# Kernel optimization log

Measured on AMD Instinct MI355X. Metric: run time of the kernel, lower is better.

## Reference

```python
import jax, jax.numpy as jnp
import numpy as np

N_SENTS, N_ENTS, BATCH, DIM, HEADS = 64, 16, 64, 512, 8


def setup_inputs() -> dict:
    key = jax.random.key(0)
    ks = jax.random.split(key, 10)
    se = N_SENTS * N_ENTS
    s = 0.02  # init scale for projection weights
    entities = jax.random.normal(ks[0], (se, BATCH, DIM), dtype=jnp.float32)
    query_param = jax.random.uniform(ks[1], (1, 1, DIM), jnp.float32, -1.0, 1.0)
    wq = jax.random.normal(ks[2], (DIM, DIM), jnp.float32) * s
    wk = jax.random.normal(ks[3], (DIM, DIM), jnp.float32) * s
    wv = jax.random.normal(ks[4], (DIM, DIM), jnp.float32) * s
    wo = jax.random.normal(ks[5], (DIM, DIM), jnp.float32) * s
    bq = jax.random.normal(ks[6], (DIM,), jnp.float32) * s
    bk = jax.random.normal(ks[7], (DIM,), jnp.float32) * s
    bv = jax.random.normal(ks[8], (DIM,), jnp.float32) * s
    bo = jax.random.normal(ks[9], (DIM,), jnp.float32) * s
    return {"entities": entities, "query_param": query_param,
            "wq": wq, "wk": wk, "wv": wv, "wo": wo,
            "bq": bq, "bk": bk, "bv": bv, "bo": bo,
            "n_sents": N_SENTS}


def reference(entities, query_param, wq, wk, wv, wo, bq, bk, bv, bo, n_sents):
    # entities: [n_sents*n_ents, batch, dim]
    se, b, d = entities.shape
    n_ents = se // n_sents
    h = HEADS
    hd = d // h

    # Learned single query broadcast to every (sentence, batch) slot.
    q_in = jnp.broadcast_to(query_param, (n_sents, b, d))
    q = q_in @ wq.T + bq            # [n_sents, b, d]
    k = entities @ wk.T + bk        # [se, b, d]
    v = entities @ wv.T + bv        # [se, b, d]

    # Split heads -> [b, h, len, hd]
    qh = q.reshape(n_sents, b, h, hd).transpose(1, 2, 0, 3)
    kh = k.reshape(se, b, h, hd).transpose(1, 2, 0, 3)
    vh = v.reshape(se, b, h, hd).transpose(1, 2, 0, 3)

    scale = jnp.asarray(1.0 / np.sqrt(hd), dtype=qh.dtype)
    scores = jnp.einsum('bhqd,bhkd->bhqk', qh, kh) * scale  # [b,h,n_sents,se]

    # Block-diagonal mask: query i attends only to keys [i*n_ents, (i+1)*n_ents)
    valid = (jnp.arange(se) // n_ents)[None, :] == jnp.arange(n_sents)[:, None]
    scores = jnp.where(valid[None, None], scores, jnp.finfo(scores.dtype).min)

    attn = jax.nn.softmax(scores, axis=-1)
    ctx = jnp.einsum('bhqk,bhkd->bhqd', attn, vh)            # [b,h,n_sents,hd]
    out = ctx.transpose(2, 0, 1, 3).reshape(n_sents, b, d)   # merge heads
    return out @ wo.T + bo                                   # [n_sents, b, d]
```

## Files before the change

kernel.cpp:

```cpp
#include <hip/hip_runtime.h>
#include <stdint.h>

#define HEADS 8
#define DIM   512
#define HD    64
#define NE    16
#define NS    64
#define NB    64

typedef short bf16x8 __attribute__((ext_vector_type(8)));
typedef float f32x4  __attribute__((ext_vector_type(4)));

__device__ __forceinline__ unsigned short f2bf(float f) {
    union { float f; uint32_t u; } v; v.f = f;
    uint32_t u = v.u;
    u += 0x7fffu + ((u >> 16) & 1u);
    return (unsigned short)(u >> 16);
}
__device__ __forceinline__ float bf_lo(uint32_t u) {
    union { uint32_t u; float f; } v; v.u = u << 16; return v.f;
}
__device__ __forceinline__ float bf_hi(uint32_t u) {
    union { uint32_t u; float f; } v; v.u = u & 0xffff0000u; return v.f;
}

__device__ __forceinline__ uint32_t cvt2(float a, float b) {
    uint32_t r;
    asm("v_cvt_pk_bf16_f32 %0, %1, %2" : "=v"(r) : "v"(a), "v"(b));
    return r;
}
__device__ __forceinline__ uint2 cvt4(float4 v) {
    return (uint2){cvt2(v.x, v.y), cvt2(v.z, v.w)};
}

__global__ __launch_bounds__(256) void k_prep(
    const float* __restrict__ qp, const float* __restrict__ wq,
    const float* __restrict__ bq, const float* __restrict__ wk,
    const float* __restrict__ wv, const float* __restrict__ wo,
    unsigned short* __restrict__ u_bf,
    unsigned short* __restrict__ wv_bf, unsigned short* __restrict__ wo_bf)
{
    const int bid = blockIdx.x;
    const int t = threadIdx.x;
    if (bid < 16) {
        const int h = bid >> 1, ch = bid & 1;
        __shared__ float qs[HD];
        {
            const int j = t >> 2, q = t & 3;
            const float* w = wq + (size_t)(h * HD + j) * DIM + q * 128;
            const float* qq = qp + q * 128;
            float a = 0.f;
            #pragma unroll 8
            for (int i = 0; i < 128; i++) a += w[i] * qq[i];
            a += __shfl_xor(a, 1);
            a += __shfl_xor(a, 2);
            if (q == 0) qs[j] = a + bq[h * HD + j];
        }
        __syncthreads();
        const int c = ch * 256 + t;
        const float* w = wk + (size_t)(h * HD) * DIM + c;
        float acc = 0.f;
        #pragma unroll 8
        for (int j = 0; j < HD; j++) acc += qs[j] * w[(size_t)j * DIM];
        u_bf[h * DIM + c] = f2bf(acc);
        u_bf[(h + 8) * DIM + c] = 0;
        return;
    }
    const bool is_v = bid < 272;
    const float* src = is_v ? wv : wo;
    unsigned short* dst = is_v ? wv_bf : wo_bf;
    const int li = ((is_v ? bid - 16 : bid - 272) * 1024 + t * 4);
    const float4 v = *(const float4*)(src + li);
    ushort4 hv;
    hv.x = f2bf(v.x); hv.y = f2bf(v.y); hv.z = f2bf(v.z); hv.w = f2bf(v.w);
    *(ushort4*)(dst + li) = hv;
}

__global__ __launch_bounds__(256, 6) void k_attn(
    const float* __restrict__ ents, const unsigned short* __restrict__ u_bf,
    unsigned short* __restrict__ weighted)
{
    __shared__ unsigned short ent[NE * DIM];
    __shared__ float attn_s[NE][8];
    const int t = threadIdx.x;
    const int bid = blockIdx.x;
    const int s = bid >> 6, b = bid & 63;

    {
        const float* base = ents + ((size_t)(s * NE) * NB + b) * DIM;
        float4 v[8];
        #pragma unroll
        for (int i = 0; i < 8; i++) {
            const int c = t + 256 * i;
            const int e = c >> 7, d4 = c & 127;
            v[i] = *(const float4*)(base + (size_t)e * (NB * DIM) + (d4 << 2));
        }
        #pragma unroll
        for (int i = 0; i < 8; i++) {
            const int c = t + 256 * i;
            const int e = c >> 7, d4 = c & 127;
            const uint2 hv = cvt4(v[i]);
            const uint32_t off = (uint32_t)((e << 10) | (d4 << 3)) ^ (uint32_t)((e & 7) << 4);
            *(uint2*)((char*)ent + off) = hv;
        }
    }
    __syncthreads();

    if (t < 64) {
        const int m = t & 15, g = t >> 4;
        const uint32_t swz = (uint32_t)((m & 7) << 4);
        const uint32_t rowb = (uint32_t)(m << 10);
        const unsigned short* urow = u_bf + m * DIM + g * 8;
        f32x4 acc = {0.f, 0.f, 0.f, 0.f};
        #pragma unroll
        for (int ks = 0; ks < 16; ks++) {
            const int kp = g * 8 + ks * 32;
            const bf16x8 af = *(const bf16x8*)((const char*)ent + ((rowb + (uint32_t)(kp << 1)) ^ swz));
            const bf16x8 bf = *(const bf16x8*)(urow + ks * 32);
            acc = __builtin_amdgcn_mfma_f32_16x16x32_bf16(af, bf, acc, 0, 0, 0);
        }
        const float scale = 0.125f;
        float s0 = acc[0]*scale, s1 = acc[1]*scale, s2 = acc[2]*scale, s3 = acc[3]*scale;
        float mx = fmaxf(fmaxf(s0, s1), fmaxf(s2, s3));
        mx = fmaxf(mx, __shfl_xor(mx, 16));
        mx = fmaxf(mx, __shfl_xor(mx, 32));
        const float p0 = __expf(s0 - mx), p1 = __expf(s1 - mx);
        const float p2 = __expf(s2 - mx), p3 = __expf(s3 - mx);
        float sm = p0 + p1 + p2 + p3;
        sm += __shfl_xor(sm, 16);
        sm += __shfl_xor(sm, 32);
        const float inv = 1.f / sm;
        if (m < HEADS) {
            attn_s[4 * g + 0][m] = p0 * inv;
            attn_s[4 * g + 1][m] = p1 * inv;
            attn_s[4 * g + 2][m] = p2 * inv;
            attn_s[4 * g + 3][m] = p3 * inv;
        }
    }
    __syncthreads();

    {
        const int d0 = t << 1;
        unsigned short* wrow = weighted + ((size_t)bid << 12) + d0;
        #pragma unroll
        for (int hp = 0; hp < 2; hp++) {
            float accx[4], accy[4];
            #pragma unroll
            for (int h = 0; h < 4; h++) { accx[h] = 0.f; accy[h] = 0.f; }
            #pragma unroll
            for (int e = 0; e < NE; e++) {
                const uint32_t off = (uint32_t)((e << 10) | (d0 << 1)) ^ (uint32_t)((e & 7) << 4);
                const uint32_t rv = *(const uint32_t*)((const char*)ent + off);
                const float ev0 = bf_lo(rv), ev1 = bf_hi(rv);
                const f32x4 a = *(const f32x4*)&attn_s[e][hp * 4];
                accx[0] += a.x * ev0; accy[0] += a.x * ev1;
                accx[1] += a.y * ev0; accy[1] += a.y * ev1;
                accx[2] += a.z * ev0; accy[2] += a.z * ev1;
                accx[3] += a.w * ev0; accy[3] += a.w * ev1;
            }
            #pragma unroll
            for (int h = 0; h < 4; h++) {
                *(uint32_t*)(wrow + (hp * 4 + h) * DIM) = cvt2(accx[h], accy[h]);
            }
        }
    }
}

template <typename CT>
__global__ __launch_bounds__(256) void k_gemm(
    const unsigned short* __restrict__ A, int lda, int aOffY,
    const unsigned short* __restrict__ B, int ldb, int bOffY,
    const float* __restrict__ bias, CT* __restrict__ C, int ldc, int cOffY, int K)
{
    __shared__ unsigned short a_s[64][72];
    __shared__ unsigned short b_s[64][72];
    const int t = threadIdx.x;
    const int m0 = blockIdx.x * 64;
    const int y  = blockIdx.y;
    const int w = t >> 6, l = t & 63;
    const int m = l & 15, g = l >> 4;
    const int lr = t >> 2, lk = (t & 3) * 16;

    const unsigned short* Ap = A + (size_t)(m0 + lr) * lda + (size_t)aOffY * y;
    const unsigned short* Bp = B + (size_t)(bOffY * y + lr) * ldb;

    f32x4 acc[4];
    #pragma unroll
    for (int i = 0; i < 4; i++) acc[i] = (f32x4){0.f, 0.f, 0.f, 0.f};

    for (int k0 = 0; k0 < K; k0 += 64) {
        const ushort4 av0 = *(const ushort4*)(Ap + k0 + lk);
        const ushort4 av1 = *(const ushort4*)(Ap + k0 + lk + 4);
        const ushort4 av2 = *(const ushort4*)(Ap + k0 + lk + 8);
        const ushort4 av3 = *(const ushort4*)(Ap + k0 + lk + 12);
        const ushort4 bv0 = *(const ushort4*)(Bp + k0 + lk);
        const ushort4 bv1 = *(const ushort4*)(Bp + k0 + lk + 4);
        const ushort4 bv2 = *(const ushort4*)(Bp + k0 + lk + 8);
        const ushort4 bv3 = *(const ushort4*)(Bp + k0 + lk + 12);
        *(ushort4*)&a_s[lr][lk]      = av0;
        *(ushort4*)&a_s[lr][lk + 4]  = av1;
        *(ushort4*)&a_s[lr][lk + 8]  = av2;
        *(ushort4*)&a_s[lr][lk + 12] = av3;
        *(ushort4*)&b_s[lr][lk]      = bv0;
        *(ushort4*)&b_s[lr][lk + 4]  = bv1;
        *(ushort4*)&b_s[lr][lk + 8]  = bv2;
        *(ushort4*)&b_s[lr][lk + 12] = bv3;
        __syncthreads();
        #pragma unroll
        for (int kk = 0; kk < 64; kk += 32) {
            const int kp = kk + g * 8;
            const bf16x8 af = *(const bf16x8*)&a_s[w * 16 + m][kp];
            const bf16x8 b0 = *(const bf16x8*)&b_s[ 0 + m][kp];
            const bf16x8 b1 = *(const bf16x8*)&b_s[16 + m][kp];
            const bf16x8 b2 = *(const bf16x8*)&b_s[32 + m][kp];
            const bf16x8 b3 = *(const bf16x8*)&b_s[48 + m][kp];
            acc[0] = __builtin_amdgcn_mfma_f32_16x16x32_bf16(af, b0, acc[0], 0, 0, 0);
            acc[1] = __builtin_amdgcn_mfma_f32_16x16x32_bf16(af, b1, acc[1], 0, 0, 0);
            acc[2] = __builtin_amdgcn_mfma_f32_16x16x32_bf16(af, b2, acc[2], 0, 0, 0);
            acc[3] = __builtin_amdgcn_mfma_f32_16x16x32_bf16(af, b3, acc[3], 0, 0, 0);
        }
        __syncthreads();
    }

    const int colbase = cOffY * y;
    #pragma unroll
    for (int nt = 0; nt < 4; nt++) {
        const int col = colbase + nt * 16 + m;
        const float bs = bias[col];
        #pragma unroll
        for (int j = 0; j < 4; j++) {
            const int row = m0 + w * 16 + g * 4 + j;
            const float val = acc[nt][j] + bs;
            if (sizeof(CT) == 2) {
                ((unsigned short*)C)[(size_t)row * ldc + col] = f2bf(val);
            } else {
                ((float*)C)[(size_t)row * ldc + col] = val;
            }
        }
    }
}

extern "C" void kernel_launch(void* const* d_in, const int* in_sizes, int n_in,
                              void* d_out, int out_size, void* d_ws, size_t ws_size,
                              hipStream_t stream)
{
    const float* ents = (const float*)d_in[0];
    const float* qp   = (const float*)d_in[1];
    const float* wq   = (const float*)d_in[2];
    const float* wk   = (const float*)d_in[3];
    const float* wv   = (const float*)d_in[4];
    const float* wo   = (const float*)d_in[5];
    const float* bq   = (const float*)d_in[6];
    const float* bv   = (const float*)d_in[8];
    const float* bo   = (const float*)d_in[9];

    char* ws = (char*)d_ws;
    unsigned short* u_bf     = (unsigned short*)ws;
    unsigned short* wv_bf    = (unsigned short*)(ws + 65536);
    unsigned short* wo_bf    = (unsigned short*)(ws + 65536 + 524288);
    unsigned short* weighted = (unsigned short*)(ws + 2097152);
    unsigned short* ctx      = (unsigned short*)(ws + 2097152 + 33554432);

    k_prep <<<528, 256, 0, stream>>>(qp, wq, bq, wk, wv, wo, u_bf, wv_bf, wo_bf);
    k_attn <<<4096, 256, 0, stream>>>(ents, u_bf, weighted);
    k_gemm<unsigned short><<<dim3(64, 8), 256, 0, stream>>>(
        weighted, HEADS * DIM, DIM, wv_bf, DIM, HD, bv, ctx, DIM, HD, DIM);
    k_gemm<float><<<dim3(64, 8), 256, 0, stream>>>(
        ctx, DIM, 0, wo_bf, DIM, HD, bo, (float*)d_out, DIM, HD, DIM);
}
```

Baseline: 62.04 us.

## Process four batches per attention block with double-buffered entity prefetch

Each k_attn block now handles four consecutive batch indices for one sentence instead of one. It keeps a double-buffered shared-memory copy of the entities and prefetches the next batch's fp32 entity rows into registers while the current batch's scores and weighted sum are computed. The grid shrinks from 4096 to 1024 blocks and the occupancy hint drops from 6 to 4, trading parallelism for overlap of global loads with compute.

```diff
diff --git a/kernel.cpp b/kernel.cpp
--- a/kernel.cpp
+++ b/kernel.cpp
@@ -76,91 +76,109 @@
     *(ushort4*)(dst + li) = hv;
 }
 
-__global__ __launch_bounds__(256, 6) void k_attn(
+__global__ __launch_bounds__(256, 4) void k_attn(
     const float* __restrict__ ents, const unsigned short* __restrict__ u_bf,
     unsigned short* __restrict__ weighted)
 {
-    __shared__ unsigned short ent[NE * DIM];
+    __shared__ unsigned short ent[2][NE * DIM];
     __shared__ float attn_s[NE][8];
     const int t = threadIdx.x;
     const int bid = blockIdx.x;
-    const int s = bid >> 6, b = bid & 63;
-
-    {
-        const float* base = ents + ((size_t)(s * NE) * NB + b) * DIM;
-        float4 v[8];
-        #pragma unroll
-        for (int i = 0; i < 8; i++) {
-            const int c = t + 256 * i;
-            const int e = c >> 7, d4 = c & 127;
-            v[i] = *(const float4*)(base + (size_t)e * (NB * DIM) + (d4 << 2));
-        }
+    const int s = bid >> 4;
+    const int bg = (bid & 15) << 2;
+
+    const int se_ = t >> 5;
+    (void)se_;
+
+    const float* sbase = ents + ((size_t)(s * NE) * NB) * DIM;
+
+    float4 v[8];
+    #pragma unroll
+    for (int i = 0; i < 8; i++) {
+        const int c = t + 256 * i;
+        const int e = c >> 7, d4 = c & 127;
+        v[i] = *(const float4*)(sbase + ((size_t)e * NB + bg) * DIM + (d4 << 2));
+    }
+
+    for (int it = 0; it < 4; ++it) {
+        const int b = bg + it;
+        const int cur = it & 1;
+
         #pragma unroll
         for (int i = 0; i < 8; i++) {
             const int c = t + 256 * i;
             const int e = c >> 7, d4 = c & 127;
             const uint2 hv = cvt4(v[i]);
             const uint32_t off = (uint32_t)((e << 10) | (d4 << 3)) ^ (uint32_t)((e & 7) << 4);
-            *(uint2*)((char*)ent + off) = hv;
-        }
-    }
-    __syncthreads();
-
-    if (t < 64) {
-        const int m = t & 15, g = t >> 4;
-        const uint32_t swz = (uint32_t)((m & 7) << 4);
-        const uint32_t rowb = (uint32_t)(m << 10);
-        const unsigned short* urow = u_bf + m * DIM + g * 8;
-        f32x4 acc = {0.f, 0.f, 0.f, 0.f};
-        #pragma unroll
-        for (int ks = 0; ks < 16; ks++) {
-            const int kp = g * 8 + ks * 32;
-            const bf16x8 af = *(const bf16x8*)((const char*)ent + ((rowb + (uint32_t)(kp << 1)) ^ swz));
-            const bf16x8 bf = *(const bf16x8*)(urow + ks * 32);
-            acc = __builtin_amdgcn_mfma_f32_16x16x32_bf16(af, bf, acc, 0, 0, 0);
-        }
-        const float scale = 0.125f;
-        float s0 = acc[0]*scale, s1 = acc[1]*scale, s2 = acc[2]*scale, s3 = acc[3]*scale;
-        float mx = fmaxf(fmaxf(s0, s1), fmaxf(s2, s3));
-        mx = fmaxf(mx, __shfl_xor(mx, 16));
-        mx = fmaxf(mx, __shfl_xor(mx, 32));
-        const float p0 = __expf(s0 - mx), p1 = __expf(s1 - mx);
-        const float p2 = __expf(s2 - mx), p3 = __expf(s3 - mx);
-        float sm = p0 + p1 + p2 + p3;
-        sm += __shfl_xor(sm, 16);
-        sm += __shfl_xor(sm, 32);
-        const float inv = 1.f / sm;
-        if (m < HEADS) {
-            attn_s[4 * g + 0][m] = p0 * inv;
-            attn_s[4 * g + 1][m] = p1 * inv;
-            attn_s[4 * g + 2][m] = p2 * inv;
-            attn_s[4 * g + 3][m] = p3 * inv;
-        }
-    }
-    __syncthreads();
-
-    {
-        const int d0 = t << 1;
-        unsigned short* wrow = weighted + ((size_t)bid << 12) + d0;
-        #pragma unroll
-        for (int hp = 0; hp < 2; hp++) {
-            float accx[4], accy[4];
+            *(uint2*)((char*)ent[cur] + off) = hv;
+        }
+        __syncthreads();
+
+        if (it < 3) {
             #pragma unroll
-            for (int h = 0; h < 4; h++) { accx[h] = 0.f; accy[h] = 0.f; }
+            for (int i = 0; i < 8; i++) {
+                const int c = t + 256 * i;
+                const int e = c >> 7, d4 = c & 127;
+                v[i] = *(const float4*)(sbase + ((size_t)e * NB + (b + 1)) * DIM + (d4 << 2));
+            }
+        }
+
+        if (t < 64) {
+            const int m = t & 15, g = t >> 4;
+            const uint32_t swz = (uint32_t)((m & 7) << 4);
+            const uint32_t rowb = (uint32_t)(m << 10);
+            const unsigned short* urow = u_bf + m * DIM + g * 8;
+            f32x4 acc = {0.f, 0.f, 0.f, 0.f};
             #pragma unroll
-            for (int e = 0; e < NE; e++) {
-                const uint32_t off = (uint32_t)((e << 10) | (d0 << 1)) ^ (uint32_t)((e & 7) << 4);
-                const uint32_t rv = *(const uint32_t*)((const char*)ent + off);
-                const float ev0 = bf_lo(rv), ev1 = bf_hi(rv);
-                const f32x4 a = *(const f32x4*)&attn_s[e][hp * 4];
-                accx[0] += a.x * ev0; accy[0] += a.x * ev1;
-                accx[1] += a.y * ev0; accy[1] += a.y * ev1;
-                accx[2] += a.z * ev0; accy[2] += a.z * ev1;
-                accx[3] += a.w * ev0; accy[3] += a.w * ev1;
-            }
+            for (int ks = 0; ks < 16; ks++) {
+                const int kp = g * 8 + ks * 32;
+                const bf16x8 af = *(const bf16x8*)((const char*)ent[cur] + ((rowb + (uint32_t)(kp << 1)) ^ swz));
+                const bf16x8 bf = *(const bf16x8*)(urow + ks * 32);
+                acc = __builtin_amdgcn_mfma_f32_16x16x32_bf16(af, bf, acc, 0, 0, 0);
+            }
+            const float scale = 0.125f;
+            float s0 = acc[0]*scale, s1 = acc[1]*scale, s2 = acc[2]*scale, s3 = acc[3]*scale;
+            float mx = fmaxf(fmaxf(s0, s1), fmaxf(s2, s3));
+            mx = fmaxf(mx, __shfl_xor(mx, 16));
+            mx = fmaxf(mx, __shfl_xor(mx, 32));
+            const float p0 = __expf(s0 - mx), p1 = __expf(s1 - mx);
+            const float p2 = __expf(s2 - mx), p3 = __expf(s3 - mx);
+            float sm = p0 + p1 + p2 + p3;
+            sm += __shfl_xor(sm, 16);
+            sm += __shfl_xor(sm, 32);
+            const float inv = 1.f / sm;
+            if (m < HEADS) {
+                attn_s[4 * g + 0][m] = p0 * inv;
+                attn_s[4 * g + 1][m] = p1 * inv;
+                attn_s[4 * g + 2][m] = p2 * inv;
+                attn_s[4 * g + 3][m] = p3 * inv;
+            }
+        }
+        __syncthreads();
+
+        {
+            const int d0 = t << 1;
+            unsigned short* wrow = weighted + ((size_t)(s * NB + b) << 12) + d0;
             #pragma unroll
-            for (int h = 0; h < 4; h++) {
-                *(uint32_t*)(wrow + (hp * 4 + h) * DIM) = cvt2(accx[h], accy[h]);
+            for (int hp = 0; hp < 2; hp++) {
+                float accx[4], accy[4];
+                #pragma unroll
+                for (int h = 0; h < 4; h++) { accx[h] = 0.f; accy[h] = 0.f; }
+                #pragma unroll
+                for (int e = 0; e < NE; e++) {
+                    const uint32_t off = (uint32_t)((e << 10) | (d0 << 1)) ^ (uint32_t)((e & 7) << 4);
+                    const uint32_t rv = *(const uint32_t*)((const char*)ent[cur] + off);
+                    const float ev0 = bf_lo(rv), ev1 = bf_hi(rv);
+                    const f32x4 a = *(const f32x4*)&attn_s[e][hp * 4];
+                    accx[0] += a.x * ev0; accy[0] += a.x * ev1;
+                    accx[1] += a.y * ev0; accy[1] += a.y * ev1;
+                    accx[2] += a.z * ev0; accy[2] += a.z * ev1;
+                    accx[3] += a.w * ev0; accy[3] += a.w * ev1;
+                }
+                #pragma unroll
+                for (int h = 0; h < 4; h++) {
+                    *(uint32_t*)(wrow + (hp * 4 + h) * DIM) = cvt2(accx[h], accy[h]);
+                }
             }
         }
     }
@@ -262,7 +280,7 @@
     unsigned short* ctx      = (unsigned short*)(ws + 2097152 + 33554432);
 
     k_prep <<<528, 256, 0, stream>>>(qp, wq, bq, wk, wv, wo, u_bf, wv_bf, wo_bf);
-    k_attn <<<4096, 256, 0, stream>>>(ents, u_bf, weighted);
+    k_attn <<<1024, 256, 0, stream>>>(ents, u_bf, weighted);
     k_gemm<unsigned short><<<dim3(64, 8), 256, 0, stream>>>(
         weighted, HEADS * DIM, DIM, wv_bf, DIM, HD, bv, ctx, DIM, HD, DIM);
     k_gemm<float><<<dim3(64, 8), 256, 0, stream>>>(
```

New measurement: 73.72 us. 1.19x slower.
